# Kernel optimization log

Hardware: AMD Instinct MI355X
Metric: run time of the kernel (lower is better)

## Reference

```python
import jax, jax.numpy as jnp
import numpy as np

B, S, D = 2, 2048, 1024
H = 16
HD = D // H   # 64
K = 64        # local_window / neighbors per position


def setup_inputs() -> dict:
    key = jax.random.key(0)
    k1, k2, k3, k4, k5, k6 = jax.random.split(key, 6)
    scale = 1.0 / np.sqrt(D)
    x = jax.random.normal(k1, (B, S, D), dtype=jnp.float32)
    routes = jax.random.randint(k2, (S, K), 0, S, dtype=jnp.int64)
    W_qkv = jax.random.normal(k3, (D, 3 * D), dtype=jnp.float32) * scale
    b_qkv = jnp.zeros((3 * D,), dtype=jnp.float32)
    W_proj = jax.random.normal(k4, (D, D), dtype=jnp.float32) * scale
    b_proj = jnp.zeros((D,), dtype=jnp.float32)
    return {"x": x, "W_qkv": W_qkv, "b_qkv": b_qkv,
            "W_proj": W_proj, "b_proj": b_proj, "routes": routes}


def reference(x, W_qkv, b_qkv, W_proj, b_proj, routes):
    # x: (B, S, D)
    qkv = x @ W_qkv + b_qkv                       # (B, S, 3D)
    qkv = qkv.reshape(B, S, 3, H, HD)
    q, k, v = qkv[:, :, 0], qkv[:, :, 1], qkv[:, :, 2]   # (B, S, H, HD)
    q = q.transpose(0, 2, 1, 3)                   # (B, H, S, HD)
    k = k.transpose(0, 2, 1, 3)
    v = v.transpose(0, 2, 1, 3)

    r = jnp.clip(routes, 0, S - 1)                # (S, K)
    # Gather neighbor keys/values: (B, H, S, K, HD)
    k_n = k[:, :, r, :]
    v_n = v[:, :, r, :]

    scores = jnp.einsum('bhsd,bhskd->bhsk', q, k_n) / jnp.sqrt(
        jnp.asarray(HD, dtype=q.dtype))           # (B, H, S, K)
    attn = jax.nn.softmax(scores, axis=-1)
    out = jnp.einsum('bhsk,bhskd->bhsd', attn, v_n)       # (B, H, S, HD)

    out = out.transpose(0, 2, 1, 3).reshape(B, S, D)
    return out @ W_proj + b_proj
```

## Files before the change

kernel.cpp:

```cpp
#include <hip/hip_runtime.h>
#include <stdint.h>

#define B_ 2
#define S_ 2048
#define D_ 1024
#define H_ 16
#define HD_ 64
#define K_ 64

typedef __attribute__((ext_vector_type(8))) __bf16 bf16x8v;
typedef __attribute__((ext_vector_type(4))) float f32x4;
typedef __attribute__((ext_vector_type(8))) unsigned short ushort8v;

#define GLD_LDS16(g, l)                                                        \
  __builtin_amdgcn_global_load_lds(                                            \
      (const __attribute__((address_space(1))) void*)(g),                      \
      (__attribute__((address_space(3))) void*)(l), 16, 0, 0)

__device__ __forceinline__ float bf2f(unsigned short u) {
  union { unsigned u32; float f; } c;
  c.u32 = ((unsigned)u) << 16;
  return c.f;
}
__device__ __forceinline__ unsigned short f2bf(float f) {
  union { float f; unsigned u; } c;
  c.f = f;
  unsigned u = c.u;
  u += 0x7fffu + ((u >> 16) & 1u);
  return (unsigned short)(u >> 16);
}

__global__ __launch_bounds__(256) void cast_f32_bf16(
    const float4* __restrict__ in, ushort4* __restrict__ outp, int n4) {
  int i = blockIdx.x * 256 + threadIdx.x;
  if (i >= n4) return;
  float4 v = in[i];
  ushort4 o;
  o.x = f2bf(v.x); o.y = f2bf(v.y); o.z = f2bf(v.z); o.w = f2bf(v.w);
  outp[i] = o;
}

__global__ __launch_bounds__(256) void transpose_cast(
    const float* __restrict__ W, unsigned short* __restrict__ WT, int R, int C) {
  __shared__ float tile[64][65];
  const int r0 = blockIdx.y * 64;
  const int c0 = blockIdx.x * 64;
  const int t = threadIdx.x;
#pragma unroll
  for (int i = 0; i < 16; ++i) {
    int idx = t + i * 256;
    int rr = idx >> 6, cc = idx & 63;
    tile[rr][cc] = W[(size_t)(r0 + rr) * C + c0 + cc];
  }
  __syncthreads();
#pragma unroll
  for (int i = 0; i < 16; ++i) {
    int idx = t + i * 256;
    int rr = idx >> 6, cc = idx & 63;
    WT[(size_t)(c0 + rr) * R + r0 + cc] = f2bf(tile[cc][rr]);
  }
}

template <bool OUT_F32>
__global__ __launch_bounds__(256) void gemm_bias(
    const unsigned short* __restrict__ A, const unsigned short* __restrict__ Bt,
    const float* __restrict__ bias, void* __restrict__ Cout,
    int M, int N, int Kd, int gx) {
  __shared__ unsigned short As[128 * 32];
  __shared__ unsigned short Bs[128 * 32];
  const int t = threadIdx.x;
  const int w = t >> 6;
  const int l = t & 63;

  const int nblk = (int)gridDim.x;
  int id = (int)blockIdx.x;
  id = (id & 7) * (nblk >> 3) + (id >> 3);
  const int by = id / gx;
  const int bx = id - by * gx;
  const int m0 = by * 128;
  const int n0 = bx * 128;
  const int wr = w >> 1, wc = w & 1;

  f32x4 acc[4][4] = {};

  const int srow = t >> 2;
  const int scol = (t & 3) * 8;
  char* asBase = (char*)As + w * 1024;
  char* bsBase = (char*)Bs + w * 1024;

  const int lr = l & 15;
  const int kh = (l >> 4) * 8;

  const int KT = Kd >> 5;
  for (int kt = 0; kt < KT; ++kt) {
    const int k0 = kt << 5;
    {
      const unsigned short* g0 = A + (size_t)(m0 + srow) * Kd + k0 + scol;
      const unsigned short* g1 = A + (size_t)(m0 + 64 + srow) * Kd + k0 + scol;
      GLD_LDS16(g0, asBase);
      GLD_LDS16(g1, asBase + 4096);
      const unsigned short* h0 = Bt + (size_t)(n0 + srow) * Kd + k0 + scol;
      const unsigned short* h1 = Bt + (size_t)(n0 + 64 + srow) * Kd + k0 + scol;
      GLD_LDS16(h0, bsBase);
      GLD_LDS16(h1, bsBase + 4096);
    }
    __syncthreads();
    bf16x8v af[4], bfv[4];
#pragma unroll
    for (int m = 0; m < 4; ++m)
      af[m] = *(const bf16x8v*)&As[(wr * 64 + m * 16 + lr) * 32 + kh];
#pragma unroll
    for (int n = 0; n < 4; ++n)
      bfv[n] = *(const bf16x8v*)&Bs[(wc * 64 + n * 16 + lr) * 32 + kh];
#pragma unroll
    for (int m = 0; m < 4; ++m)
#pragma unroll
      for (int n = 0; n < 4; ++n)
        acc[m][n] = __builtin_amdgcn_mfma_f32_16x16x32_bf16(af[m], bfv[n],
                                                            acc[m][n], 0, 0, 0);
    __syncthreads();
  }

  const int rbase = (l >> 4) * 4;
#pragma unroll
  for (int m = 0; m < 4; ++m) {
#pragma unroll
    for (int n = 0; n < 4; ++n) {
      const int gc = n0 + wc * 64 + n * 16 + lr;
      const float bv = bias[gc];
#pragma unroll
      for (int j = 0; j < 4; ++j) {
        const int gr = m0 + wr * 64 + m * 16 + rbase + j;
        float v = acc[m][n][j] + bv;
        if (OUT_F32)
          ((float*)Cout)[(size_t)gr * N + gc] = v;
        else
          ((unsigned short*)Cout)[(size_t)gr * N + gc] = f2bf(v);
      }
    }
  }
}

__global__ __launch_bounds__(256) void attn_kernel(
    const unsigned short* __restrict__ qkv, const int* __restrict__ routes,
    unsigned short* __restrict__ outp) {
  __shared__ unsigned rtsoff[64];
  __shared__ float pbuf[1024];
  __shared__ float lbuf[16];
  const int bs = blockIdx.x;
  const int b = bs >> 11;
  const int s = bs & (S_ - 1);
  const int t = threadIdx.x;
  const int w = t >> 6, l = t & 63;
  const int kh2 = w >> 1, hh = w & 1;

  if (t < 64) {
    int r = routes[s * K_ + t];
    r = min(max(r, 0), S_ - 1);
    rtsoff[t] = (unsigned)(b * S_ + r) * 3072u;
  }
  __syncthreads();

  const unsigned colo = hh * 512 + l * 8;
  const int head = colo >> 6;

  float q[8];
  {
    ushort8v u = *(const ushort8v*)(qkv + (size_t)bs * 3072 + colo);
#pragma unroll
    for (int i = 0; i < 8; ++i) q[i] = bf2f(u[i]);
  }

  const unsigned kofs = 1024u + colo;
  const int jbase = kh2 * 32;

  float acc[8] = {};
  float lsum = 0.f;
#pragma unroll 4
  for (int j2 = 0; j2 < 32; ++j2) {
    const unsigned ro = rtsoff[jbase + j2];
    ushort8v ku = *(const ushort8v*)(qkv + (ro + kofs));
    ushort8v vu = *(const ushort8v*)(qkv + (ro + kofs + 1024u));
    float d = q[0] * bf2f(ku[0]);
#pragma unroll
    for (int i = 1; i < 8; ++i) d += q[i] * bf2f(ku[i]);
    d += __shfl_xor(d, 1);
    d += __shfl_xor(d, 2);
    d += __shfl_xor(d, 4);
    const float p = __expf(d * 0.125f);
    lsum += p;
#pragma unroll
    for (int i = 0; i < 8; ++i) acc[i] += p * bf2f(vu[i]);
  }

  if (kh2 == 1) {
    f32x4 a0 = {acc[0], acc[1], acc[2], acc[3]};
    f32x4 a1 = {acc[4], acc[5], acc[6], acc[7]};
    *(f32x4*)&pbuf[colo] = a0;
    *(f32x4*)&pbuf[colo + 4] = a1;
    if ((l & 7) == 0) lbuf[head] = lsum;
  }
  __syncthreads();
  if (kh2 == 0) {
    const float inv = 1.0f / (lsum + lbuf[head]);
    ushort8v o;
#pragma unroll
    for (int i = 0; i < 8; ++i) o[i] = f2bf((acc[i] + pbuf[colo + i]) * inv);
    *(ushort8v*)(outp + (size_t)bs * D_ + colo) = o;
  }
}

extern "C" void kernel_launch(void* const* d_in, const int* in_sizes, int n_in,
                              void* d_out, int out_size, void* d_ws,
                              size_t ws_size, hipStream_t stream) {
  const float* x = (const float*)d_in[0];
  const float* Wqkv = (const float*)d_in[1];
  const float* bqkv = (const float*)d_in[2];
  const float* Wproj = (const float*)d_in[3];
  const float* bproj = (const float*)d_in[4];
  const int* routes = (const int*)d_in[5];
  float* out = (float*)d_out;

  char* ws = (char*)d_ws;
  unsigned short* x_bf = (unsigned short*)(ws);
  unsigned short* wqkvT = (unsigned short*)(ws + 8388608);
  unsigned short* wprojT = (unsigned short*)(ws + 14680064);
  unsigned short* qkv = (unsigned short*)(ws + 16777216);
  unsigned short* aout = (unsigned short*)(ws + 41943040);

  {
    int n4 = (B_ * S_ * D_) / 4;
    cast_f32_bf16<<<n4 / 256, 256, 0, stream>>>((const float4*)x,
                                                (ushort4*)x_bf, n4);
  }
  transpose_cast<<<dim3(3 * D_ / 64, D_ / 64), 256, 0, stream>>>(Wqkv, wqkvT,
                                                                 D_, 3 * D_);
  transpose_cast<<<dim3(D_ / 64, D_ / 64), 256, 0, stream>>>(Wproj, wprojT, D_,
                                                             D_);
  {
    int gx = 3 * D_ / 128, gy = B_ * S_ / 128;
    gemm_bias<false><<<gx * gy, 256, 0, stream>>>(x_bf, wqkvT, bqkv, qkv,
                                                  B_ * S_, 3 * D_, D_, gx);
  }
  attn_kernel<<<B_ * S_, 256, 0, stream>>>(qkv, routes, aout);
  {
    int gx = D_ / 128, gy = B_ * S_ / 128;
    gemm_bias<true><<<gx * gy, 256, 0, stream>>>(aout, wprojT, bproj, out,
                                                 B_ * S_, D_, D_, gx);
  }
}
```

Measured before the change: 161.0 us.

## Split QKV output into separate Q/K/V buffers and two-pass attention gather

The QKV GEMM now writes Q, K and V into three separate contiguous [B*S,1024] buffers instead of one interleaved 3072-wide buffer. The attention kernel gathers K rows first to compute scores, stores the exp weights in shared memory, then gathers V rows in a second loop. This packs each gathered tensor more densely, which should improve cache and TLB locality for the random route gathers. The cost is an extra shared-memory buffer and two dependent loops, which may expose more load latency per pass. The 1/sqrt(HD) scale is also folded into q.

```diff
diff --git a/kernel.cpp b/kernel.cpp
--- a/kernel.cpp
+++ b/kernel.cpp
@@ -61,11 +61,11 @@
   }
 }
 
-template <bool OUT_F32>
+template <bool OUT_F32, bool SPLIT3>
 __global__ __launch_bounds__(256) void gemm_bias(
     const unsigned short* __restrict__ A, const unsigned short* __restrict__ Bt,
-    const float* __restrict__ bias, void* __restrict__ Cout,
-    int M, int N, int Kd, int gx) {
+    const float* __restrict__ bias, void* __restrict__ C0, void* __restrict__ C1,
+    void* __restrict__ C2, int M, int N, int Kd, int gx) {
   __shared__ unsigned short As[128 * 32];
   __shared__ unsigned short Bs[128 * 32];
   const int t = threadIdx.x;
@@ -80,6 +80,19 @@
   const int m0 = by * 128;
   const int n0 = bx * 128;
   const int wr = w >> 1, wc = w & 1;
+
+  void* Cw;
+  int nb, Nout;
+  if (SPLIT3) {
+    const int rg = n0 >> 10;
+    Cw = rg == 0 ? C0 : (rg == 1 ? C1 : C2);
+    nb = n0 & 1023;
+    Nout = 1024;
+  } else {
+    Cw = C0;
+    nb = n0;
+    Nout = N;
+  }
 
   f32x4 acc[4][4] = {};
 
@@ -126,24 +139,26 @@
   for (int m = 0; m < 4; ++m) {
 #pragma unroll
     for (int n = 0; n < 4; ++n) {
-      const int gc = n0 + wc * 64 + n * 16 + lr;
-      const float bv = bias[gc];
+      const int gcb = wc * 64 + n * 16 + lr;
+      const float bv = bias[n0 + gcb];
 #pragma unroll
       for (int j = 0; j < 4; ++j) {
         const int gr = m0 + wr * 64 + m * 16 + rbase + j;
         float v = acc[m][n][j] + bv;
         if (OUT_F32)
-          ((float*)Cout)[(size_t)gr * N + gc] = v;
+          ((float*)Cw)[(size_t)gr * Nout + nb + gcb] = v;
         else
-          ((unsigned short*)Cout)[(size_t)gr * N + gc] = f2bf(v);
+          ((unsigned short*)Cw)[(size_t)gr * Nout + nb + gcb] = f2bf(v);
       }
     }
   }
 }
 
 __global__ __launch_bounds__(256) void attn_kernel(
-    const unsigned short* __restrict__ qkv, const int* __restrict__ routes,
+    const unsigned short* __restrict__ qb, const unsigned short* __restrict__ kb,
+    const unsigned short* __restrict__ vb, const int* __restrict__ routes,
     unsigned short* __restrict__ outp) {
+  __shared__ float sc[16][68];
   __shared__ unsigned rtsoff[64];
   __shared__ float pbuf[1024];
   __shared__ float lbuf[16];
@@ -157,7 +172,7 @@
   if (t < 64) {
     int r = routes[s * K_ + t];
     r = min(max(r, 0), S_ - 1);
-    rtsoff[t] = (unsigned)(b * S_ + r) * 3072u;
+    rtsoff[t] = (unsigned)(b * S_ + r) * 1024u;
   }
   __syncthreads();
 
@@ -166,31 +181,37 @@
 
   float q[8];
   {
-    ushort8v u = *(const ushort8v*)(qkv + (size_t)bs * 3072 + colo);
-#pragma unroll
-    for (int i = 0; i < 8; ++i) q[i] = bf2f(u[i]);
-  }
-
-  const unsigned kofs = 1024u + colo;
+    ushort8v u = *(const ushort8v*)(qb + (size_t)bs * 1024 + colo);
+#pragma unroll
+    for (int i = 0; i < 8; ++i) q[i] = bf2f(u[i]) * 0.125f;
+  }
+
   const int jbase = kh2 * 32;
 
-  float acc[8] = {};
   float lsum = 0.f;
 #pragma unroll 4
   for (int j2 = 0; j2 < 32; ++j2) {
-    const unsigned ro = rtsoff[jbase + j2];
-    ushort8v ku = *(const ushort8v*)(qkv + (ro + kofs));
-    ushort8v vu = *(const ushort8v*)(qkv + (ro + kofs + 1024u));
+    const int j = jbase + j2;
+    ushort8v ku = *(const ushort8v*)(kb + (rtsoff[j] + colo));
     float d = q[0] * bf2f(ku[0]);
 #pragma unroll
     for (int i = 1; i < 8; ++i) d += q[i] * bf2f(ku[i]);
     d += __shfl_xor(d, 1);
     d += __shfl_xor(d, 2);
     d += __shfl_xor(d, 4);
-    const float p = __expf(d * 0.125f);
+    const float p = __expf(d);
     lsum += p;
-#pragma unroll
-    for (int i = 0; i < 8; ++i) acc[i] += p * bf2f(vu[i]);
+    sc[head][j] = p;
+  }
+
+  float acc[8] = {};
+#pragma unroll 4
+  for (int j2 = 0; j2 < 32; ++j2) {
+    const int j = jbase + j2;
+    ushort8v vu = *(const ushort8v*)(vb + (rtsoff[j] + colo));
+    const float pw = sc[head][j];
+#pragma unroll
+    for (int i = 0; i < 8; ++i) acc[i] += pw * bf2f(vu[i]);
   }
 
   if (kh2 == 1) {
@@ -225,7 +246,9 @@
   unsigned short* x_bf = (unsigned short*)(ws);
   unsigned short* wqkvT = (unsigned short*)(ws + 8388608);
   unsigned short* wprojT = (unsigned short*)(ws + 14680064);
-  unsigned short* qkv = (unsigned short*)(ws + 16777216);
+  unsigned short* q_buf = (unsigned short*)(ws + 16777216);
+  unsigned short* k_buf = (unsigned short*)(ws + 25165824);
+  unsigned short* v_buf = (unsigned short*)(ws + 33554432);
   unsigned short* aout = (unsigned short*)(ws + 41943040);
 
   {
@@ -239,13 +262,13 @@
                                                              D_);
   {
     int gx = 3 * D_ / 128, gy = B_ * S_ / 128;
-    gemm_bias<false><<<gx * gy, 256, 0, stream>>>(x_bf, wqkvT, bqkv, qkv,
-                                                  B_ * S_, 3 * D_, D_, gx);
-  }
-  attn_kernel<<<B_ * S_, 256, 0, stream>>>(qkv, routes, aout);
+    gemm_bias<false, true><<<gx * gy, 256, 0, stream>>>(
+        x_bf, wqkvT, bqkv, q_buf, k_buf, v_buf, B_ * S_, 3 * D_, D_, gx);
+  }
+  attn_kernel<<<B_ * S_, 256, 0, stream>>>(q_buf, k_buf, v_buf, routes, aout);
   {
     int gx = D_ / 128, gy = B_ * S_ / 128;
-    gemm_bias<true><<<gx * gy, 256, 0, stream>>>(aout, wprojT, bproj, out,
-                                                 B_ * S_, D_, D_, gx);
-  }
-}
+    gemm_bias<true, false><<<gx * gy, 256, 0, stream>>>(
+        aout, wprojT, bproj, out, nullptr, nullptr, B_ * S_, D_, D_, gx);
+  }
+}
```

Result: faster. 157.1 us (-2.4%).

## Split attention into score and value passes, drop GEMM block swizzle

Applied to the files above, without the earlier changes.

The attention kernel now computes all exp scores first, stores them in shared memory, synchronises, and then gathers V rows in a second loop. The 1/sqrt(HD) scale is folded into q. Separately, the GEMMs drop the XCD-aware block-id remapping and use a plain 2D grid. The split adds a barrier and shared-memory traffic, and it also stops K and V loads from overlapping in the same iteration. Removing the swizzle may hurt L2 locality across the chiplets.

```diff
diff --git a/kernel.cpp b/kernel.cpp
--- a/kernel.cpp
+++ b/kernel.cpp
@@ -65,20 +65,14 @@
 __global__ __launch_bounds__(256) void gemm_bias(
     const unsigned short* __restrict__ A, const unsigned short* __restrict__ Bt,
     const float* __restrict__ bias, void* __restrict__ Cout,
-    int M, int N, int Kd, int gx) {
+    int M, int N, int Kd) {
   __shared__ unsigned short As[128 * 32];
   __shared__ unsigned short Bs[128 * 32];
   const int t = threadIdx.x;
   const int w = t >> 6;
   const int l = t & 63;
-
-  const int nblk = (int)gridDim.x;
-  int id = (int)blockIdx.x;
-  id = (id & 7) * (nblk >> 3) + (id >> 3);
-  const int by = id / gx;
-  const int bx = id - by * gx;
-  const int m0 = by * 128;
-  const int n0 = bx * 128;
+  const int m0 = blockIdx.y * 128;
+  const int n0 = blockIdx.x * 128;
   const int wr = w >> 1, wc = w & 1;
 
   f32x4 acc[4][4] = {};
@@ -144,6 +138,7 @@
 __global__ __launch_bounds__(256) void attn_kernel(
     const unsigned short* __restrict__ qkv, const int* __restrict__ routes,
     unsigned short* __restrict__ outp) {
+  __shared__ float sc[16][68];
   __shared__ unsigned rtsoff[64];
   __shared__ float pbuf[1024];
   __shared__ float lbuf[16];
@@ -168,29 +163,39 @@
   {
     ushort8v u = *(const ushort8v*)(qkv + (size_t)bs * 3072 + colo);
 #pragma unroll
-    for (int i = 0; i < 8; ++i) q[i] = bf2f(u[i]);
+    for (int i = 0; i < 8; ++i) q[i] = bf2f(u[i]) * 0.125f;
   }
 
   const unsigned kofs = 1024u + colo;
+  const unsigned vofs = 2048u + colo;
   const int jbase = kh2 * 32;
 
-  float acc[8] = {};
   float lsum = 0.f;
 #pragma unroll 4
   for (int j2 = 0; j2 < 32; ++j2) {
-    const unsigned ro = rtsoff[jbase + j2];
-    ushort8v ku = *(const ushort8v*)(qkv + (ro + kofs));
-    ushort8v vu = *(const ushort8v*)(qkv + (ro + kofs + 1024u));
+    const int j = jbase + j2;
+    ushort8v ku = *(const ushort8v*)(qkv + (rtsoff[j] + kofs));
     float d = q[0] * bf2f(ku[0]);
 #pragma unroll
     for (int i = 1; i < 8; ++i) d += q[i] * bf2f(ku[i]);
     d += __shfl_xor(d, 1);
     d += __shfl_xor(d, 2);
     d += __shfl_xor(d, 4);
-    const float p = __expf(d * 0.125f);
+    const float p = __expf(d);
     lsum += p;
-#pragma unroll
-    for (int i = 0; i < 8; ++i) acc[i] += p * bf2f(vu[i]);
+    sc[head][j] = p;
+  }
+
+  __syncthreads();
+
+  float acc[8] = {};
+#pragma unroll 4
+  for (int j2 = 0; j2 < 32; ++j2) {
+    const int j = jbase + j2;
+    ushort8v vu = *(const ushort8v*)(qkv + (rtsoff[j] + vofs));
+    const float pw = sc[head][j];
+#pragma unroll
+    for (int i = 0; i < 8; ++i) acc[i] += pw * bf2f(vu[i]);
   }
 
   if (kh2 == 1) {
@@ -237,15 +242,9 @@
                                                                  D_, 3 * D_);
   transpose_cast<<<dim3(D_ / 64, D_ / 64), 256, 0, stream>>>(Wproj, wprojT, D_,
                                                              D_);
-  {
-    int gx = 3 * D_ / 128, gy = B_ * S_ / 128;
-    gemm_bias<false><<<gx * gy, 256, 0, stream>>>(x_bf, wqkvT, bqkv, qkv,
-                                                  B_ * S_, 3 * D_, D_, gx);
-  }
+  gemm_bias<false><<<dim3(3 * D_ / 128, B_ * S_ / 128), 256, 0, stream>>>(
+      x_bf, wqkvT, bqkv, qkv, B_ * S_, 3 * D_, D_);
   attn_kernel<<<B_ * S_, 256, 0, stream>>>(qkv, routes, aout);
-  {
-    int gx = D_ / 128, gy = B_ * S_ / 128;
-    gemm_bias<true><<<gx * gy, 256, 0, stream>>>(aout, wprojT, bproj, out,
-                                                 B_ * S_, D_, D_, gx);
-  }
-}
+  gemm_bias<true><<<dim3(D_ / 128, B_ * S_ / 128), 256, 0, stream>>>(
+      aout, wprojT, bproj, out, B_ * S_, D_, D_);
+}
```

After: 159.9 us. About the same (-0.7%).
